# Kernel tuning notes

Hardware: AMD Instinct MI355X
Metric: run time of the kernel (lower is better)

## Reference

```python
import jax, jax.numpy as jnp
import numpy as np
from jax import lax

N_RAYS, N_STEPS, G = 4096, 160, 160
COLOR_DIM, WIDTH = 3, 128
POS_PE, VIEW_PE = 5, 4
XYZ_MIN, XYZ_MAX = -1.0, 1.0
NEAR = 0.05
STEPSIZE = 0.5
VOXEL_SIZE = (XYZ_MAX - XYZ_MIN) / G
DIST = STEPSIZE * VOXEL_SIZE
S_VAL = 80.0
FASTCOLOR_THRES = 1e-7
MASK_THRES = 1e-3
ALPHA_INIT = 1e-4
ACT_SHIFT = float(np.log(1.0 / (1.0 - ALPHA_INIT) - 1.0))
SMOOTH_K, SMOOTH_SIGMA = 5, 1.0
POSFREQ = jnp.asarray([2.0 ** i for i in range(POS_PE)], jnp.float32)
VIEWFREQ = jnp.asarray([2.0 ** i for i in range(VIEW_PE)], jnp.float32)


def _gauss_kernel():
    ax = np.arange(SMOOTH_K) - SMOOTH_K // 2
    g = np.exp(-(ax ** 2) / (2.0 * SMOOTH_SIGMA ** 2))
    k = g[:, None, None] * g[None, :, None] * g[None, None, :]
    return jnp.asarray(k / k.sum(), np.float32)[None, None]


def _trilerp(grid, pts):
    # grid [C,Gx,Gx,Gx]; pts [...,3] in world coords -> [..., C] (align_corners trilinear)
    Gx = grid.shape[-1]
    u = (pts - XYZ_MIN) / (XYZ_MAX - XYZ_MIN) * (Gx - 1)
    u = jnp.clip(u, 0.0, Gx - 1.0)
    i0 = jnp.clip(jnp.floor(u).astype(jnp.int32), 0, Gx - 2)
    f = u - i0.astype(u.dtype)
    x0, y0, z0 = i0[..., 0], i0[..., 1], i0[..., 2]
    fx, fy, fz = f[..., 0], f[..., 1], f[..., 2]
    def g8(ix, iy, iz):
        return grid[:, ix, iy, iz]  # [C, ...]
    out = (g8(x0, y0, z0) * (1 - fx) * (1 - fy) * (1 - fz)
         + g8(x0, y0, z0 + 1) * (1 - fx) * (1 - fy) * fz
         + g8(x0, y0 + 1, z0) * (1 - fx) * fy * (1 - fz)
         + g8(x0, y0 + 1, z0 + 1) * (1 - fx) * fy * fz
         + g8(x0 + 1, y0, z0) * fx * (1 - fy) * (1 - fz)
         + g8(x0 + 1, y0, z0 + 1) * fx * (1 - fy) * fz
         + g8(x0 + 1, y0 + 1, z0) * fx * fy * (1 - fz)
         + g8(x0 + 1, y0 + 1, z0 + 1) * fx * fy * fz)
    return jnp.moveaxis(out, 0, -1)


def _alphas2weights(alpha):
    # per-ray (segmented) exclusive cumprod of transmittance; alpha [N,S]
    T = jnp.cumprod(1.0 - alpha, axis=1)
    T_excl = jnp.concatenate([jnp.ones_like(T[:, :1]), T[:, :-1]], axis=1)
    return alpha * T_excl, T[:, -1]


def _mlp(x, w0, b0, w1, b1, w2, b2):
    h = jax.nn.relu(x @ w0 + b0)
    h = jax.nn.relu(h @ w1 + b1)
    return h @ w2 + b2


def _forward(rays_o, rays_d, viewdirs, sdf_grid, mask_density,
             off_color_grid, emo_color_grid,
             off_w0, off_b0, off_w1, off_b1, off_w2, off_b2,
             emo_w0, emo_b0, emo_w1, emo_b1, emo_w2, emo_b2, em_modes):
    N = rays_o.shape[0]
    t = NEAR + DIST * jnp.arange(N_STEPS, dtype=jnp.float32)
    ray_pts = rays_o[:, None, :] + rays_d[:, None, :] * t[None, :, None]  # [N,S,3]

    # MaskCache: threshold alpha from coarse density grid (boolean keep mask)
    dens = _trilerp(mask_density, ray_pts)[..., 0]
    mask_alpha = 1.0 - jnp.exp(-jax.nn.softplus(dens + ACT_SHIFT) * DIST)
    keep0 = mask_alpha >= MASK_THRES  # [N,S]

    # Gaussian-smoothed SDF grid + central-difference gradient grid
    sdf_s = lax.conv_general_dilated(sdf_grid, _gauss_kernel(), (1, 1, 1), 'SAME',
                                     dimension_numbers=('NCDHW', 'OIDHW', 'NCDHW'))[0]  # [1,G,G,G]
    s = sdf_s[0]
    grad_grid = jnp.zeros((3, G, G, G), sdf_grid.dtype)
    grad_grid = grad_grid.at[0, 1:-1].set((s[2:] - s[:-2]) / (2 * VOXEL_SIZE))
    grad_grid = grad_grid.at[1, :, 1:-1].set((s[:, 2:] - s[:, :-2]) / (2 * VOXEL_SIZE))
    grad_grid = grad_grid.at[2, :, :, 1:-1].set((s[:, :, 2:] - s[:, :, :-2]) / (2 * VOXEL_SIZE))

    sdf = _trilerp(sdf_s, ray_pts)[..., 0]   # [N,S]
    gradient = _trilerp(grad_grid, ray_pts)  # [N,S,3]

    # NeuS alpha from sdf (scatter, grad variant, cos_anneal = 1)
    true_cos = jnp.einsum('nd,nsd->ns', viewdirs, gradient)
    iter_cos = -jax.nn.relu(-true_cos)
    prev_cdf = jax.nn.sigmoid((sdf - iter_cos * DIST * 0.5) * S_VAL)
    next_cdf = jax.nn.sigmoid((sdf + iter_cos * DIST * 0.5) * S_VAL)
    alpha = jnp.clip((prev_cdf - next_cdf + 1e-5) / (prev_cdf + 1e-5), 0.0, 1.0)
    alpha = jnp.where(keep0, alpha, 0.0)  # masked points contribute nothing

    weights, _ = _alphas2weights(alpha)
    keep1 = weights > FASTCOLOR_THRES
    alpha = jnp.where(keep1, alpha, 0.0)
    weights, alphainv_last = _alphas2weights(alpha)

    # features: pos PE, view PE (per-ray, gathered by ray_id == broadcast), normal
    rays_xyz = (ray_pts - XYZ_MIN) / (XYZ_MAX - XYZ_MIN)  # [N,S,3]
    xyz_emb = (rays_xyz[..., None] * POSFREQ).reshape(N, N_STEPS, -1)
    v_emb = (viewdirs[..., None] * VIEWFREQ).reshape(N, -1)
    v_full = jnp.concatenate([v_emb, jnp.sin(v_emb), jnp.cos(v_emb)], -1)
    v_full = jnp.broadcast_to(v_full[:, None, :], (N, N_STEPS, v_full.shape[-1]))
    normal = gradient / (jnp.linalg.norm(gradient, axis=-1, keepdims=True) + 1e-5)
    rgb_feat = jnp.concatenate([rays_xyz, jnp.sin(xyz_emb), jnp.cos(xyz_emb), v_full, normal], -1)

    off_in = jnp.concatenate([_trilerp(off_color_grid, ray_pts), rgb_feat], -1)
    emo_in = jnp.concatenate([_trilerp(emo_color_grid, ray_pts), rgb_feat], -1)
    off_rgb = jax.nn.sigmoid(_mlp(off_in, off_w0, off_b0, off_w1, off_b1, off_w2, off_b2))
    emo_rgb = jax.nn.sigmoid(_mlp(emo_in, emo_w0, emo_b0, emo_w1, emo_b1, emo_w2, emo_b2))
    on_mask = (em_modes == 1)[:, None, None]  # em_modes[ray_id] == 1
    rgb = jnp.where(on_mask, emo_rgb, 0.0) + off_rgb

    w_ = weights[..., None]
    rgb_marched = jnp.sum(w_ * rgb, axis=1)  # segment_coo(sum over ray_id)
    cum_weights = jnp.sum(w_, axis=1)        # [N,1]
    return rgb_marched, alphainv_last, 1.0 - cum_weights


def setup_inputs() -> dict:
    key = jax.random.key(0)
    ks = jax.random.split(key, 12)
    rays_o = jax.random.uniform(ks[0], (N_RAYS, 3), jnp.float32, -0.3, 0.3)
    rd = jax.random.normal(ks[1], (N_RAYS, 3), jnp.float32)
    rays_d = rd / jnp.linalg.norm(rd, axis=-1, keepdims=True)
    viewdirs = rays_d
    em_modes = jax.random.randint(ks[2], (N_RAYS,), 0, 2)
    lin = np.linspace(-1.0, 1.0, G, dtype=np.float32)
    x, y, z = np.meshgrid(lin, lin, lin, indexing='ij')
    sdf_grid = jnp.asarray(np.sqrt(x ** 2 + y ** 2 + z ** 2) - 1.0)[None, None]  # sphere-SDF init
    mask_density = jax.random.normal(ks[3], (1, 80, 80, 80), jnp.float32) * 2.0 + 12.0
    off_color_grid = jax.random.normal(ks[4], (COLOR_DIM, G, G, G), jnp.float32) * 0.1
    emo_color_grid = jax.random.normal(ks[5], (COLOR_DIM, G, G, G), jnp.float32) * 0.1
    DIM0 = 3 + 3 * POS_PE * 2 + 3 * VIEW_PE * 3 + COLOR_DIM + 3  # = 75
    def lw(k, i, o):
        return jax.random.normal(k, (i, o), jnp.float32) * (1.0 / np.sqrt(i))
    return dict(rays_o=rays_o, rays_d=rays_d, viewdirs=viewdirs, em_modes=em_modes,
                sdf_grid=sdf_grid, mask_density=mask_density,
                off_color_grid=off_color_grid, emo_color_grid=emo_color_grid,
                off_w0=lw(ks[6], DIM0, WIDTH), off_b0=jnp.zeros((WIDTH,), jnp.float32),
                off_w1=lw(ks[7], WIDTH, WIDTH), off_b1=jnp.zeros((WIDTH,), jnp.float32),
                off_w2=lw(ks[8], WIDTH, 3), off_b2=jnp.zeros((3,), jnp.float32),
                emo_w0=lw(ks[9], DIM0, WIDTH), emo_b0=jnp.zeros((WIDTH,), jnp.float32),
                emo_w1=lw(ks[10], WIDTH, WIDTH), emo_b1=jnp.zeros((WIDTH,), jnp.float32),
                emo_w2=lw(ks[11], WIDTH, 3), emo_b2=jnp.zeros((3,), jnp.float32))


def reference(rays_o, rays_d, viewdirs, em_modes, sdf_grid, mask_density,
              off_color_grid, emo_color_grid,
              off_w0, off_b0, off_w1, off_b1, off_w2, off_b2,
              emo_w0, emo_b0, emo_w1, emo_b1, emo_w2, emo_b2):
    return _forward(rays_o, rays_d, viewdirs, sdf_grid, mask_density,
                    off_color_grid, emo_color_grid,
                    off_w0, off_b0, off_w1, off_b1, off_w2, off_b2,
                    emo_w0, emo_b0, emo_w1, emo_b1, emo_w2, emo_b2, em_modes)
```

## Files before the change

### kernel.cpp

```cpp
#include <hip/hip_runtime.h>

#define NRAYS 4096
#define NSTEPS 160
#define NSAMP (NRAYS*NSTEPS)
#define GG 160
#define GG2 (GG*GG)
#define GG3 (GG*GG2)
#define GM 80
#define GM2 (GM*GM)

#define NEARV 0.05f
#define DISTV 0.00625f
#define SVAL 80.0f
#define ACT_SHIFT_C (-9.2102403669758813f)
#define INV2H 40.0f
#define MASK_THRES_C 1e-3f
#define FAST_THRES_C 1e-7f

#define KW0 0.05448868454964295f
#define KW1 0.24420134200323332f
#define KW2 0.40261994689424750f

__device__ __forceinline__ float sigmf(float x){ return 1.0f/(1.0f+__expf(-x)); }
__device__ __forceinline__ float softplusf_(float x){ return (x>20.0f)? x : log1pf(__expf(x)); }

__device__ __forceinline__ void tricoord(float p, int Gx, int& i0, float& fr){
  float u = (p + 1.0f)*0.5f*(float)(Gx-1);
  u = fminf(fmaxf(u, 0.0f), (float)(Gx-1));
  int i = (int)floorf(u);
  i = min(max(i,0), Gx-2);
  i0 = i; fr = u - (float)i;
}

__global__ __launch_bounds__(256) void ksmooth_yz(const float* __restrict__ in, float* __restrict__ out,
                                                  float* __restrict__ outbuf, int* __restrict__ cnt){
  __shared__ float S[36][37];
  __shared__ float Tz[36][33];
  const int bx = blockIdx.x;
  const int t = threadIdx.x;
  if (bx == 0){
    for (int i = t; i < NRAYS*3; i += 256) outbuf[i] = 0.0f;
    if (t < 2) cnt[t] = 0;
  }
  const int x  = bx / 25;
  const int tile = bx % 25;
  const int Y0 = (tile/5)*32, Z0 = (tile%5)*32;
  const float kw[5] = {KW0,KW1,KW2,KW1,KW0};
  for (int i = t; i < 36*36; i += 256){
    int r = i/36, c = i - (i/36)*36;
    int y = Y0 + r - 2, z = Z0 + c - 2;
    float v = 0.0f;
    if (y>=0 && y<GG && z>=0 && z<GG) v = in[(x*GG+y)*GG+z];
    S[r][c] = v;
  }
  __syncthreads();
  for (int i = t; i < 36*32; i += 256){
    int r = i >> 5, c = i & 31;
    float acc = 0.f;
    #pragma unroll
    for (int d=0; d<5; d++) acc += kw[d]*S[r][c+d];
    Tz[r][c] = acc;
  }
  __syncthreads();
  for (int i = t; i < 32*32; i += 256){
    int yy = i >> 5, c = i & 31;
    float acc = 0.f;
    #pragma unroll
    for (int d=0; d<5; d++) acc += kw[d]*Tz[yy+d][c];
    out[(x*GG + Y0+yy)*GG + Z0 + c] = acc;
  }
}

__global__ __launch_bounds__(64) void kmarch(
  const float* __restrict__ ro, const float* __restrict__ rd,
  const float* __restrict__ vd, const int* __restrict__ em,
  const float* __restrict__ maskg, const float* __restrict__ Y,
  int* __restrict__ slist, float* __restrict__ sw, float* __restrict__ sgrad,
  int* __restrict__ cnt, float* __restrict__ out)
{
  int n = blockIdx.x*64 + threadIdx.x;
  if (n >= NRAYS) return;
  const float ox=ro[n*3+0], oy=ro[n*3+1], oz=ro[n*3+2];
  const float dx=rd[n*3+0], dy=rd[n*3+1], dz=rd[n*3+2];
  const float vx=vd[n*3+0], vy=vd[n*3+1], vz=vd[n*3+2];
  const int emn = em[n];
  const float kwc[5] = {KW0,KW1,KW2,KW1,KW0};
  float T1=1.0f, T2=1.0f, cum=0.0f;
  for (int s=0; s<NSTEPS; s++){
    float tt = NEARV + DISTV*(float)s;
    float px = ox + dx*tt, py = oy + dy*tt, pz = oz + dz*tt;

    int mx,my,mz; float mfx,mfy,mfz;
    tricoord(px, GM, mx, mfx); tricoord(py, GM, my, mfy); tricoord(pz, GM, mz, mfz);
    int mid = (mx*GM + my)*GM + mz;
    float d000=maskg[mid],        d001=maskg[mid+1];
    float d010=maskg[mid+GM],     d011=maskg[mid+GM+1];
    float d100=maskg[mid+GM2],    d101=maskg[mid+GM2+1];
    float d110=maskg[mid+GM2+GM], d111=maskg[mid+GM2+GM+1];
    float m00 = d000 + (d001-d000)*mfz;
    float m01 = d010 + (d011-d010)*mfz;
    float m10 = d100 + (d101-d100)*mfz;
    float m11 = d110 + (d111-d110)*mfz;
    float m0 = m00 + (m01-m00)*mfy;
    float m1 = m10 + (m11-m10)*mfy;
    float dens = m0 + (m1-m0)*mfx;
    float malpha = 1.0f - __expf(-softplusf_(dens + ACT_SHIFT_C)*DISTV);

    int ix,iy,iz; float fx,fy,fz;
    tricoord(px, GG, ix, fx); tricoord(py, GG, iy, fy); tricoord(pz, GG, iz, fz);

    float R[2][2][8];
    #pragma unroll
    for (int jb=0;jb<2;jb++)
      #pragma unroll
      for (int jc=0;jc<2;jc++)
        #pragma unroll
        for (int j=0;j<8;j++){
          int a = ix-3+j;
          R[jb][jc][j] = (a>=0 && a<GG) ? Y[(a*GG + iy+jb)*GG + iz+jc] : 0.0f;
        }
    const bool hasym = (iy>=1), hasyp = (iy<=GG-3);
    const bool haszm = (iz>=1), haszp = (iz<=GG-3);
    float Eym[2][6], Eyp[2][6], Ezm[2][6], Ezp[2][6];
    #pragma unroll
    for (int jc=0;jc<2;jc++)
      #pragma unroll
      for (int j=0;j<6;j++){
        int a = ix-2+j;
        bool ax = (a>=0 && a<GG);
        Eym[jc][j] = (hasym && ax) ? Y[(a*GG + iy-1)*GG + iz+jc] : 0.0f;
        Eyp[jc][j] = (hasyp && ax) ? Y[(a*GG + iy+2)*GG + iz+jc] : 0.0f;
      }
    #pragma unroll
    for (int jb=0;jb<2;jb++)
      #pragma unroll
      for (int j=0;j<6;j++){
        int a = ix-2+j;
        bool ax = (a>=0 && a<GG);
        Ezm[jb][j] = (haszm && ax) ? Y[(a*GG + iy+jb)*GG + iz-1] : 0.0f;
        Ezp[jb][j] = (haszp && ax) ? Y[(a*GG + iy+jb)*GG + iz+2] : 0.0f;
      }

    float sdf=0.0f, gx=0.0f, gy=0.0f, gz=0.0f;
    #pragma unroll
    for (int ja=0;ja<2;ja++){
      #pragma unroll
      for (int jb=0;jb<2;jb++){
        #pragma unroll
        for (int jc=0;jc<2;jc++){
          float w = (ja?fx:1.0f-fx)*(jb?fy:1.0f-fy)*(jc?fz:1.0f-fz);
          const float* r = R[jb][jc];
          float s0=0.0f;
          #pragma unroll
          for (int t2=0;t2<5;t2++) s0 += kwc[t2]*r[ja+1+t2];
          sdf += w*s0;
          int a = ix+ja, b = iy+jb, c = iz+jc;
          if (a>=1 && a<=GG-2){
            float sp=0.0f, sm=0.0f;
            #pragma unroll
            for (int t2=0;t2<5;t2++){ sp += kwc[t2]*r[ja+2+t2]; sm += kwc[t2]*r[ja+t2]; }
            gx += w*INV2H*(sp-sm);
          }
          if (b>=1 && b<=GG-2){
            float acc=0.0f;
            if (jb==0){
              const float* up = R[1][jc];
              const float* dn = Eym[jc];
              #pragma unroll
              for (int t2=0;t2<5;t2++) acc += kwc[t2]*(up[ja+1+t2] - dn[ja+t2]);
            } else {
              const float* up = Eyp[jc];
              const float* dn = R[0][jc];
              #pragma unroll
              for (int t2=0;t2<5;t2++) acc += kwc[t2]*(up[ja+t2] - dn[ja+1+t2]);
            }
            gy += w*INV2H*acc;
          }
          if (c>=1 && c<=GG-2){
            float acc=0.0f;
            if (jc==0){
              const float* up = R[jb][1];
              const float* dn = Ezm[jb];
              #pragma unroll
              for (int t2=0;t2<5;t2++) acc += kwc[t2]*(up[ja+1+t2] - dn[ja+t2]);
            } else {
              const float* up = Ezp[jb];
              const float* dn = R[jb][0];
              #pragma unroll
              for (int t2=0;t2<5;t2++) acc += kwc[t2]*(up[ja+t2] - dn[ja+1+t2]);
            }
            gz += w*INV2H*acc;
          }
        }
      }
    }

    float tc = vx*gx + vy*gy + vz*gz;
    float icos = fminf(tc, 0.0f);
    float e = icos*DISTV*0.5f;
    float prev = sigmf((sdf - e)*SVAL);
    float nxt  = sigmf((sdf + e)*SVAL);
    float alpha = (prev - nxt + 1e-5f)/(prev + 1e-5f);
    alpha = fminf(fmaxf(alpha, 0.0f), 1.0f);
    if (!(malpha >= MASK_THRES_C)) alpha = 0.0f;

    float w1 = alpha*T1; T1 *= (1.0f - alpha);
    float a2 = (w1 > FAST_THRES_C) ? alpha : 0.0f;
    float wv = a2*T2;   T2 *= (1.0f - a2);
    cum += wv;
    if (wv > 0.0f){
      int pos;
      if (emn == 1){ int p = atomicAdd(&cnt[1], 1); pos = NSAMP - 1 - p; }
      else         { pos = atomicAdd(&cnt[0], 1); }
      slist[pos] = n*NSTEPS + s;
      sw[pos] = wv;
      sgrad[pos*3+0]=gx; sgrad[pos*3+1]=gy; sgrad[pos*3+2]=gz;
    }
    if (T1 <= FAST_THRES_C) break;
  }
  out[NRAYS*3 + n] = T2;
  out[NRAYS*4 + n] = 1.0f - cum;
}

#define DO4(ACC, XV) \
  ACC.x += XV.x*w0.x; ACC.y += XV.x*w0.y; ACC.z += XV.x*w0.z; ACC.w += XV.x*w0.w; \
  ACC.x += XV.y*w1.x; ACC.y += XV.y*w1.y; ACC.z += XV.y*w1.z; ACC.w += XV.y*w1.w; \
  ACC.x += XV.z*w2.x; ACC.y += XV.z*w2.y; ACC.z += XV.z*w2.z; ACC.w += XV.z*w2.w; \
  ACC.x += XV.w*w3.x; ACC.y += XV.w*w3.y; ACC.z += XV.w*w3.z; ACC.w += XV.w*w3.w;

__global__ __launch_bounds__(256, 1) void kmlp8(
  const float* __restrict__ ro, const float* __restrict__ rd,
  const float* __restrict__ vd,
  const float* __restrict__ offc, const float* __restrict__ emoc,
  const int* __restrict__ slist, const float* __restrict__ sw,
  const float* __restrict__ sgrad, const int* __restrict__ cnt,
  const float* __restrict__ W0o, const float* __restrict__ b0o,
  const float* __restrict__ W1o, const float* __restrict__ b1o,
  const float* __restrict__ W2o, const float* __restrict__ b2o,
  const float* __restrict__ W0e, const float* __restrict__ b0e,
  const float* __restrict__ W1e, const float* __restrict__ b1e,
  const float* __restrict__ W2e, const float* __restrict__ b2e,
  float* __restrict__ out)
{
  __shared__ float X [4][8][80];
  __shared__ float HA[4][8][128];
  __shared__ float HB[4][8][128];
  __shared__ float SW_[4][8];
  __shared__ int   SS_[4][8];

  const int t = threadIdx.x;
  const int wid = t >> 6;
  const int lt  = t & 63;
  const int c0 = cnt[0], c1 = cnt[1];
  const int seg1 = NSAMP - c1;
  const int totOff = c0 + c1;
  const int nOff = (totOff + 7) >> 3;
  const int nEmo = (c1 + 7) >> 3;
  const int nTask = nOff + nEmo;

  for (int task = blockIdx.x*4 + wid; task < nTask; task += gridDim.x*4) {
    const int head = (task >= nOff) ? 1 : 0;
    const int total = head ? c1 : totOff;
    const int base = (head ? (task - nOff) : task) * 8;

    const float* W0 = head ? W0e : W0o;  const float* b0 = head ? b0e : b0o;
    const float* W1 = head ? W1e : W1o;  const float* b1 = head ? b1e : b1o;
    const float* W2 = head ? W2e : W2o;  const float* b2 = head ? b2e : b2o;
    const float* cg = head ? emoc : offc;
    const float4* W04 = (const float4*)W0;
    const float4* W14 = (const float4*)W1;

    {
      const int s = lt >> 3;
      const int r = lt & 7;
      int v = base + s;
      bool vld = (v < total);
      int vc = vld ? v : (total > 0 ? total - 1 : 0);
      int gi = head ? (seg1 + vc) : ((vc < c0) ? vc : seg1 + (vc - c0));
      const int samp = slist[gi];
      if (r == 0){
        SS_[wid][s] = samp;
        SW_[wid][s] = vld ? sw[gi] : 0.0f;
      }
      const int n = samp / NSTEPS;
      const int step = samp - n*NSTEPS;
      const float tt = NEARV + DISTV*(float)step;
      const float px = ro[n*3+0] + rd[n*3+0]*tt;
      const float py = ro[n*3+1] + rd[n*3+1]*tt;
      const float pz = ro[n*3+2] + rd[n*3+2]*tt;
      float* Xs = X[wid][s];
      if (r < 3) {
        int ix,iy,iz; float fx,fy,fz;
        tricoord(px, GG, ix, fx); tricoord(py, GG, iy, fy); tricoord(pz, GG, iz, fz);
        const float* g = cg + (size_t)r * GG3;
        const int id = (ix*GG + iy)*GG + iz;
        float v000=g[id],        v001=g[id+1];
        float v010=g[id+GG],     v011=g[id+GG+1];
        float v100=g[id+GG2],    v101=g[id+GG2+1];
        float v110=g[id+GG2+GG], v111=g[id+GG2+GG+1];
        float c00 = v000 + (v001-v000)*fz;
        float c01 = v010 + (v011-v010)*fz;
        float c10 = v100 + (v101-v100)*fz;
        float c11 = v110 + (v111-v110)*fz;
        float cl0 = c00 + (c01-c00)*fy;
        float cl1 = c10 + (c11-c10)*fy;
        Xs[r] = cl0 + (cl1-cl0)*fx;
      } else if (r == 3) {
        Xs[3] = (px+1.0f)*0.5f;
        Xs[4] = (py+1.0f)*0.5f;
        Xs[5] = (pz+1.0f)*0.5f;
        float gx = sgrad[gi*3+0], gy = sgrad[gi*3+1], gz = sgrad[gi*3+2];
        float inv = 1.0f/(sqrtf(gx*gx+gy*gy+gz*gz)+1e-5f);
        Xs[72] = gx*inv; Xs[73] = gy*inv; Xs[74] = gz*inv;
        Xs[75] = 0.0f; Xs[76] = 0.0f; Xs[77] = 0.0f; Xs[78] = 0.0f; Xs[79] = 0.0f;
      } else if (r < 7) {
        const int a = r - 4;
        const float coord = (a==0)?px:((a==1)?py:pz);
        const float rxyz = (coord+1.0f)*0.5f;
        float fr = 1.0f;
        #pragma unroll
        for (int q = 0; q < 5; q++) {
          float e = rxyz*fr; fr *= 2.0f;
          Xs[6  + a*5 + q] = __sinf(e);
          Xs[21 + a*5 + q] = __cosf(e);
        }
      } else {
        #pragma unroll
        for (int a = 0; a < 3; a++){
          const float vv = vd[n*3+a];
          float fr = 1.0f;
          #pragma unroll
          for (int q = 0; q < 4; q++) {
            float e = vv*fr; fr *= 2.0f;
            Xs[36 + a*4 + q] = e;
            Xs[48 + a*4 + q] = __sinf(e);
            Xs[60 + a*4 + q] = __cosf(e);
          }
        }
      }
    }

    const int sme = lt >> 5;
    const int l32 = lt & 31;
    const int sb = sme*4;

    {
      const float4 bb = ((const float4*)b0)[l32];
      float4 a0 = bb, a1 = bb, a2 = bb, a3 = bb;
      const float* X0 = X[wid][sb+0];
      const float* X1 = X[wid][sb+1];
      const float* X2 = X[wid][sb+2];
      const float* X3 = X[wid][sb+3];
      #pragma unroll 2
      for (int k4 = 0; k4 < 72; k4 += 4){
        float4 w0 = W04[(k4+0)*32 + l32];
        float4 w1 = W04[(k4+1)*32 + l32];
        float4 w2 = W04[(k4+2)*32 + l32];
        float4 w3 = W04[(k4+3)*32 + l32];
        float4 x0 = *(const float4*)&X0[k4];
        float4 x1 = *(const float4*)&X1[k4];
        float4 x2 = *(const float4*)&X2[k4];
        float4 x3 = *(const float4*)&X3[k4];
        DO4(a0, x0); DO4(a1, x1); DO4(a2, x2); DO4(a3, x3);
      }
      #pragma unroll
      for (int k = 72; k < 75; k++){
        float4 w = W04[k*32 + l32];
        float x0 = X0[k], x1 = X1[k], x2 = X2[k], x3 = X3[k];
        a0.x+=x0*w.x; a0.y+=x0*w.y; a0.z+=x0*w.z; a0.w+=x0*w.w;
        a1.x+=x1*w.x; a1.y+=x1*w.y; a1.z+=x1*w.z; a1.w+=x1*w.w;
        a2.x+=x2*w.x; a2.y+=x2*w.y; a2.z+=x2*w.z; a2.w+=x2*w.w;
        a3.x+=x3*w.x; a3.y+=x3*w.y; a3.z+=x3*w.z; a3.w+=x3*w.w;
      }
      a0.x=fmaxf(a0.x,0.f); a0.y=fmaxf(a0.y,0.f); a0.z=fmaxf(a0.z,0.f); a0.w=fmaxf(a0.w,0.f);
      a1.x=fmaxf(a1.x,0.f); a1.y=fmaxf(a1.y,0.f); a1.z=fmaxf(a1.z,0.f); a1.w=fmaxf(a1.w,0.f);
      a2.x=fmaxf(a2.x,0.f); a2.y=fmaxf(a2.y,0.f); a2.z=fmaxf(a2.z,0.f); a2.w=fmaxf(a2.w,0.f);
      a3.x=fmaxf(a3.x,0.f); a3.y=fmaxf(a3.y,0.f); a3.z=fmaxf(a3.z,0.f); a3.w=fmaxf(a3.w,0.f);
      *(float4*)&HA[wid][sb+0][l32*4] = a0;
      *(float4*)&HA[wid][sb+1][l32*4] = a1;
      *(float4*)&HA[wid][sb+2][l32*4] = a2;
      *(float4*)&HA[wid][sb+3][l32*4] = a3;
    }

    {
      const float4 bb = ((const float4*)b1)[l32];
      float4 a0 = bb, a1 = bb, a2 = bb, a3 = bb;
      const float* H0 = HA[wid][sb+0];
      const float* H1 = HA[wid][sb+1];
      const float* H2p = HA[wid][sb+2];
      const float* H3 = HA[wid][sb+3];
      #pragma unroll 2
      for (int k4 = 0; k4 < 128; k4 += 4){
        float4 w0 = W14[(k4+0)*32 + l32];
        float4 w1 = W14[(k4+1)*32 + l32];
        float4 w2 = W14[(k4+2)*32 + l32];
        float4 w3 = W14[(k4+3)*32 + l32];
        float4 x0 = *(const float4*)&H0[k4];
        float4 x1 = *(const float4*)&H1[k4];
        float4 x2 = *(const float4*)&H2p[k4];
        float4 x3 = *(const float4*)&H3[k4];
        DO4(a0, x0); DO4(a1, x1); DO4(a2, x2); DO4(a3, x3);
      }
      a0.x=fmaxf(a0.x,0.f); a0.y=fmaxf(a0.y,0.f); a0.z=fmaxf(a0.z,0.f); a0.w=fmaxf(a0.w,0.f);
      a1.x=fmaxf(a1.x,0.f); a1.y=fmaxf(a1.y,0.f); a1.z=fmaxf(a1.z,0.f); a1.w=fmaxf(a1.w,0.f);
      a2.x=fmaxf(a2.x,0.f); a2.y=fmaxf(a2.y,0.f); a2.z=fmaxf(a2.z,0.f); a2.w=fmaxf(a2.w,0.f);
      a3.x=fmaxf(a3.x,0.f); a3.y=fmaxf(a3.y,0.f); a3.z=fmaxf(a3.z,0.f); a3.w=fmaxf(a3.w,0.f);
      *(float4*)&HB[wid][sb+0][l32*4] = a0;
      *(float4*)&HB[wid][sb+1][l32*4] = a1;
      *(float4*)&HB[wid][sb+2][l32*4] = a2;
      *(float4*)&HB[wid][sb+3][l32*4] = a3;
    }

    {
      float W2r[4][3];
      #pragma unroll
      for (int q = 0; q < 4; q++){
        W2r[q][0] = W2[(l32*4+q)*3+0];
        W2r[q][1] = W2[(l32*4+q)*3+1];
        W2r[q][2] = W2[(l32*4+q)*3+2];
      }
      #pragma unroll
      for (int m = 0; m < 4; m++){
        const int s = sb + m;
        float4 h = *(const float4*)&HB[wid][s][l32*4];
        float c0v = h.x*W2r[0][0] + h.y*W2r[1][0] + h.z*W2r[2][0] + h.w*W2r[3][0];
        float c1v = h.x*W2r[0][1] + h.y*W2r[1][1] + h.z*W2r[2][1] + h.w*W2r[3][1];
        float c2v = h.x*W2r[0][2] + h.y*W2r[1][2] + h.z*W2r[2][2] + h.w*W2r[3][2];
        #pragma unroll
        for (int d=16; d>=1; d>>=1){
          c0v += __shfl_down(c0v, d, 32);
          c1v += __shfl_down(c1v, d, 32);
          c2v += __shfl_down(c2v, d, 32);
        }
        if (l32 == 0){
          float w = SW_[wid][s];
          if (w > 0.0f){
            int n2 = SS_[wid][s] / NSTEPS;
            atomicAdd(&out[n2*3+0], w * sigmf(c0v + b2[0]));
            atomicAdd(&out[n2*3+1], w * sigmf(c1v + b2[1]));
            atomicAdd(&out[n2*3+2], w * sigmf(c2v + b2[2]));
          }
        }
      }
    }
  }
}

extern "C" void kernel_launch(void* const* d_in, const int* in_sizes, int n_in,
                              void* d_out, int out_size, void* d_ws, size_t ws_size,
                              hipStream_t stream) {
  const float* ro    = (const float*)d_in[0];
  const float* rd    = (const float*)d_in[1];
  const float* vd    = (const float*)d_in[2];
  const int*   em    = (const int*)d_in[3];
  const float* sdfg  = (const float*)d_in[4];
  const float* maskg = (const float*)d_in[5];
  const float* offc  = (const float*)d_in[6];
  const float* emoc  = (const float*)d_in[7];
  const float* W0o = (const float*)d_in[8];
  const float* b0o = (const float*)d_in[9];
  const float* W1o = (const float*)d_in[10];
  const float* b1o = (const float*)d_in[11];
  const float* W2o = (const float*)d_in[12];
  const float* b2o = (const float*)d_in[13];
  const float* W0e = (const float*)d_in[14];
  const float* b0e = (const float*)d_in[15];
  const float* W1e = (const float*)d_in[16];
  const float* b1e = (const float*)d_in[17];
  const float* W2e = (const float*)d_in[18];
  const float* b2e = (const float*)d_in[19];

  float* out = (float*)d_out;
  float* ws  = (float*)d_ws;
  float* Yb    = ws;
  float* swb   = ws + GG3;
  float* sgradb= swb + NSAMP;
  int*   slist = (int*)(sgradb + 3*(size_t)NSAMP);
  int*   cnt   = slist + NSAMP;

  ksmooth_yz<<<GG*25, 256, 0, stream>>>(sdfg, Yb, out, cnt);

  kmarch<<<NRAYS/64, 64, 0, stream>>>(ro, rd, vd, em, maskg, Yb,
                                      slist, swb, sgradb, cnt, out);

  kmlp8<<<256, 256, 0, stream>>>(ro, rd, vd, offc, emoc,
                                 slist, swb, sgradb, cnt,
                                 W0o,b0o,W1o,b1o,W2o,b2o,
                                 W0e,b0e,W1e,b1e,W2e,b2e, out);
}
```

Baseline: 54.32 us.

## March each ray with a full wavefront, distributing stencil loads across lanes

The ray-march kernel now assigns one 64-lane wavefront per ray instead of one thread per ray. Each lane fetches one of the ~88 smoothed-SDF stencil values or one of the 8 mask-grid corners and computes a partial weighted contribution. Five butterfly shuffle reductions then combine the sdf, gradient and density terms. This exposes far more parallelism: 4096 rays previously gave only 64 blocks of 64 threads. The cost is serial per-step shuffle reductions and 64x redundant scalar transmittance logic per ray.

Result: slower. 87.74 us (+61.5%).

```diff
diff --git a/kernel.cpp b/kernel.cpp
--- a/kernel.cpp
+++ b/kernel.cpp
@@ -23,6 +23,12 @@
 
 __device__ __forceinline__ float sigmf(float x){ return 1.0f/(1.0f+__expf(-x)); }
 __device__ __forceinline__ float softplusf_(float x){ return (x>20.0f)? x : log1pf(__expf(x)); }
+
+__device__ __forceinline__ float kwf(int i){
+  float r = 0.0f;
+  r = (i==0)?KW0:r; r=(i==1)?KW1:r; r=(i==2)?KW2:r; r=(i==3)?KW1:r; r=(i==4)?KW0:r;
+  return r;
+}
 
 __device__ __forceinline__ void tricoord(float p, int Gx, int& i0, float& fr){
   float u = (p + 1.0f)*0.5f*(float)(Gx-1);
@@ -71,155 +77,137 @@
   }
 }
 
-__global__ __launch_bounds__(64) void kmarch(
+__global__ __launch_bounds__(256) void kmarch_wave(
   const float* __restrict__ ro, const float* __restrict__ rd,
   const float* __restrict__ vd, const int* __restrict__ em,
   const float* __restrict__ maskg, const float* __restrict__ Y,
   int* __restrict__ slist, float* __restrict__ sw, float* __restrict__ sgrad,
   int* __restrict__ cnt, float* __restrict__ out)
 {
-  int n = blockIdx.x*64 + threadIdx.x;
+  const int t = threadIdx.x;
+  const int l = t & 63;
+  const int n = blockIdx.x*4 + (t>>6);
   if (n >= NRAYS) return;
+
   const float ox=ro[n*3+0], oy=ro[n*3+1], oz=ro[n*3+2];
   const float dx=rd[n*3+0], dy=rd[n*3+1], dz=rd[n*3+2];
   const float vx=vd[n*3+0], vy=vd[n*3+1], vz=vd[n*3+2];
   const int emn = em[n];
-  const float kwc[5] = {KW0,KW1,KW2,KW1,KW0};
+
+  const bool isR = (l < 32);
+  const bool isE = (l >= 32 && l < 56);
+  const bool isM = (l >= 56);
+  const int r_jb = (l>>4)&1, r_jc = (l>>3)&1, r_u = l&7;
+  const int e1 = l-32, e_wh = e1/12, e_r = e1%12, e_jc = e_r/6, e_u = e_r%6;
+  const int mb = l-56, m_ca=(mb>>2)&1, m_cb=(mb>>1)&1, m_cc=mb&1;
+  const bool isZ = (l < 24);
+  const int z_wh = l/12, z_r = l%12, z_jb = z_r/6, z_u = z_r%6;
+
+  const float kA = kwf(r_u-1), kB = kwf(r_u-2), kC = kwf(r_u), kD = kwf(r_u-3);
+  const float dG1 = kB - kC, dG2 = kD - kA;
+  const float kE = kwf(e_u), kF = kwf(e_u-1);
+  const float kZ1 = kwf(z_u), kZ2 = kwf(z_u-1);
+
   float T1=1.0f, T2=1.0f, cum=0.0f;
   for (int s=0; s<NSTEPS; s++){
-    float tt = NEARV + DISTV*(float)s;
-    float px = ox + dx*tt, py = oy + dy*tt, pz = oz + dz*tt;
+    const float tt = NEARV + DISTV*(float)s;
+    const float px = ox + dx*tt, py = oy + dy*tt, pz = oz + dz*tt;
 
     int mx,my,mz; float mfx,mfy,mfz;
     tricoord(px, GM, mx, mfx); tricoord(py, GM, my, mfy); tricoord(pz, GM, mz, mfz);
-    int mid = (mx*GM + my)*GM + mz;
-    float d000=maskg[mid],        d001=maskg[mid+1];
-    float d010=maskg[mid+GM],     d011=maskg[mid+GM+1];
-    float d100=maskg[mid+GM2],    d101=maskg[mid+GM2+1];
-    float d110=maskg[mid+GM2+GM], d111=maskg[mid+GM2+GM+1];
-    float m00 = d000 + (d001-d000)*mfz;
-    float m01 = d010 + (d011-d010)*mfz;
-    float m10 = d100 + (d101-d100)*mfz;
-    float m11 = d110 + (d111-d110)*mfz;
-    float m0 = m00 + (m01-m00)*mfy;
-    float m1 = m10 + (m11-m10)*mfy;
-    float dens = m0 + (m1-m0)*mfx;
-    float malpha = 1.0f - __expf(-softplusf_(dens + ACT_SHIFT_C)*DISTV);
-
     int ix,iy,iz; float fx,fy,fz;
     tricoord(px, GG, ix, fx); tricoord(py, GG, iy, fy); tricoord(pz, GG, iz, fz);
 
-    float R[2][2][8];
+    const float ax0 = (ix>=1)?1.f:0.f, ax1 = (ix<=GG-3)?1.f:0.f;
+    const float by0f = (iy>=1)?1.f:0.f, by1f = (iy<=GG-3)?1.f:0.f;
+    const float bz0f = (iz>=1)?1.f:0.f, bz1f = (iz<=GG-3)?1.f:0.f;
+    const float wx0=1.f-fx, wx1=fx, wy0=1.f-fy, wy1=fy, wz0=1.f-fz, wz1=fz;
+
+    float V1 = 0.0f, V2 = 0.0f;
+    if (isR){
+      int a = ix-3+r_u;
+      if (a>=0 && a<GG) V1 = Y[(a*GG + iy+r_jb)*GG + iz+r_jc];
+    } else if (isE){
+      int a = ix-2+e_u;
+      int b = e_wh ? (iy+2) : (iy-1);
+      bool ok = (a>=0 && a<GG) && (e_wh ? (iy<=GG-3) : (iy>=1));
+      if (ok) V1 = Y[(a*GG + b)*GG + iz+e_jc];
+    } else {
+      V1 = maskg[((mx+m_ca)*GM + my+m_cb)*GM + mz+m_cc];
+    }
+    if (isZ){
+      int a = ix-2+z_u;
+      int c = z_wh ? (iz+2) : (iz-1);
+      bool ok = (a>=0 && a<GG) && (z_wh ? (iz<=GG-3) : (iz>=1));
+      if (ok) V2 = Y[(a*GG + iy+z_jb)*GG + c];
+    }
+
+    float p_sdf=0.f, p_gx=0.f, p_gy=0.f, p_gz=0.f, p_den=0.f;
+    if (isR){
+      const float wyv = r_jb ? wy1 : wy0;
+      const float wzv = r_jc ? wz1 : wz0;
+      const float cxs = wx0*kA + wx1*kB;
+      const float cgx = wx0*ax0*dG1 + wx1*ax1*dG2;
+      const float base = wzv*cxs*INV2H*V1;
+      p_sdf = wyv*wzv*cxs*V1;
+      p_gx  = wyv*wzv*cgx*V1*INV2H;
+      p_gy  = base * (r_jb ? (wy0*by0f) : -(wy1*by1f));
+      p_gz  = wyv*cxs*INV2H*V1 * (r_jc ? (wz0*bz0f) : -(wz1*bz1f));
+    } else if (isE){
+      const float wzv = e_jc ? wz1 : wz0;
+      const float cxe = wx0*kE + wx1*kF;
+      const float gyw = e_wh ? (wy1*by1f) : -(wy0*by0f);
+      p_gy = wzv*cxe*INV2H*gyw*V1;
+    } else {
+      const float wmx = m_ca? mfx : 1.f-mfx;
+      const float wmy = m_cb? mfy : 1.f-mfy;
+      const float wmz = m_cc? mfz : 1.f-mfz;
+      p_den = wmx*wmy*wmz*V1;
+    }
+    if (isZ){
+      const float wyv = z_jb ? wy1 : wy0;
+      const float cxe2 = wx0*kZ1 + wx1*kZ2;
+      const float gzw = z_wh ? (wz1*bz1f) : -(wz0*bz0f);
+      p_gz += wyv*cxe2*INV2H*gzw*V2;
+    }
+
     #pragma unroll
-    for (int jb=0;jb<2;jb++)
-      #pragma unroll
-      for (int jc=0;jc<2;jc++)
-        #pragma unroll
-        for (int j=0;j<8;j++){
-          int a = ix-3+j;
-          R[jb][jc][j] = (a>=0 && a<GG) ? Y[(a*GG + iy+jb)*GG + iz+jc] : 0.0f;
-        }
-    const bool hasym = (iy>=1), hasyp = (iy<=GG-3);
-    const bool haszm = (iz>=1), haszp = (iz<=GG-3);
-    float Eym[2][6], Eyp[2][6], Ezm[2][6], Ezp[2][6];
-    #pragma unroll
-    for (int jc=0;jc<2;jc++)
-      #pragma unroll
-      for (int j=0;j<6;j++){
-        int a = ix-2+j;
-        bool ax = (a>=0 && a<GG);
-        Eym[jc][j] = (hasym && ax) ? Y[(a*GG + iy-1)*GG + iz+jc] : 0.0f;
-        Eyp[jc][j] = (hasyp && ax) ? Y[(a*GG + iy+2)*GG + iz+jc] : 0.0f;
-      }
-    #pragma unroll
-    for (int jb=0;jb<2;jb++)
-      #pragma unroll
-      for (int j=0;j<6;j++){
-        int a = ix-2+j;
-        bool ax = (a>=0 && a<GG);
-        Ezm[jb][j] = (haszm && ax) ? Y[(a*GG + iy+jb)*GG + iz-1] : 0.0f;
-        Ezp[jb][j] = (haszp && ax) ? Y[(a*GG + iy+jb)*GG + iz+2] : 0.0f;
-      }
-
-    float sdf=0.0f, gx=0.0f, gy=0.0f, gz=0.0f;
-    #pragma unroll
-    for (int ja=0;ja<2;ja++){
-      #pragma unroll
-      for (int jb=0;jb<2;jb++){
-        #pragma unroll
-        for (int jc=0;jc<2;jc++){
-          float w = (ja?fx:1.0f-fx)*(jb?fy:1.0f-fy)*(jc?fz:1.0f-fz);
-          const float* r = R[jb][jc];
-          float s0=0.0f;
-          #pragma unroll
-          for (int t2=0;t2<5;t2++) s0 += kwc[t2]*r[ja+1+t2];
-          sdf += w*s0;
-          int a = ix+ja, b = iy+jb, c = iz+jc;
-          if (a>=1 && a<=GG-2){
-            float sp=0.0f, sm=0.0f;
-            #pragma unroll
-            for (int t2=0;t2<5;t2++){ sp += kwc[t2]*r[ja+2+t2]; sm += kwc[t2]*r[ja+t2]; }
-            gx += w*INV2H*(sp-sm);
-          }
-          if (b>=1 && b<=GG-2){
-            float acc=0.0f;
-            if (jb==0){
-              const float* up = R[1][jc];
-              const float* dn = Eym[jc];
-              #pragma unroll
-              for (int t2=0;t2<5;t2++) acc += kwc[t2]*(up[ja+1+t2] - dn[ja+t2]);
-            } else {
-              const float* up = Eyp[jc];
-              const float* dn = R[0][jc];
-              #pragma unroll
-              for (int t2=0;t2<5;t2++) acc += kwc[t2]*(up[ja+t2] - dn[ja+1+t2]);
-            }
-            gy += w*INV2H*acc;
-          }
-          if (c>=1 && c<=GG-2){
-            float acc=0.0f;
-            if (jc==0){
-              const float* up = R[jb][1];
-              const float* dn = Ezm[jb];
-              #pragma unroll
-              for (int t2=0;t2<5;t2++) acc += kwc[t2]*(up[ja+1+t2] - dn[ja+t2]);
-            } else {
-              const float* up = Ezp[jb];
-              const float* dn = R[jb][0];
-              #pragma unroll
-              for (int t2=0;t2<5;t2++) acc += kwc[t2]*(up[ja+t2] - dn[ja+1+t2]);
-            }
-            gz += w*INV2H*acc;
-          }
-        }
-      }
-    }
-
-    float tc = vx*gx + vy*gy + vz*gz;
-    float icos = fminf(tc, 0.0f);
-    float e = icos*DISTV*0.5f;
-    float prev = sigmf((sdf - e)*SVAL);
-    float nxt  = sigmf((sdf + e)*SVAL);
+    for (int d=1; d<64; d<<=1){
+      p_sdf += __shfl_xor(p_sdf, d, 64);
+      p_gx  += __shfl_xor(p_gx , d, 64);
+      p_gy  += __shfl_xor(p_gy , d, 64);
+      p_gz  += __shfl_xor(p_gz , d, 64);
+      p_den += __shfl_xor(p_den, d, 64);
+    }
+
+    const float malpha = 1.0f - __expf(-softplusf_(p_den + ACT_SHIFT_C)*DISTV);
+    const float tc = vx*p_gx + vy*p_gy + vz*p_gz;
+    const float icos = fminf(tc, 0.0f);
+    const float e = icos*DISTV*0.5f;
+    const float prev = sigmf((p_sdf - e)*SVAL);
+    const float nxt  = sigmf((p_sdf + e)*SVAL);
     float alpha = (prev - nxt + 1e-5f)/(prev + 1e-5f);
     alpha = fminf(fmaxf(alpha, 0.0f), 1.0f);
     if (!(malpha >= MASK_THRES_C)) alpha = 0.0f;
 
-    float w1 = alpha*T1; T1 *= (1.0f - alpha);
-    float a2 = (w1 > FAST_THRES_C) ? alpha : 0.0f;
-    float wv = a2*T2;   T2 *= (1.0f - a2);
+    const float w1 = alpha*T1; T1 *= (1.0f - alpha);
+    const float a2 = (w1 > FAST_THRES_C) ? alpha : 0.0f;
+    const float wv = a2*T2;   T2 *= (1.0f - a2);
     cum += wv;
-    if (wv > 0.0f){
+    if (wv > 0.0f && l == 0){
       int pos;
       if (emn == 1){ int p = atomicAdd(&cnt[1], 1); pos = NSAMP - 1 - p; }
       else         { pos = atomicAdd(&cnt[0], 1); }
       slist[pos] = n*NSTEPS + s;
       sw[pos] = wv;
-      sgrad[pos*3+0]=gx; sgrad[pos*3+1]=gy; sgrad[pos*3+2]=gz;
+      sgrad[pos*3+0]=p_gx; sgrad[pos*3+1]=p_gy; sgrad[pos*3+2]=p_gz;
     }
     if (T1 <= FAST_THRES_C) break;
   }
-  out[NRAYS*3 + n] = T2;
-  out[NRAYS*4 + n] = 1.0f - cum;
+  if (l == 0){
+    out[NRAYS*3 + n] = T2;
+    out[NRAYS*4 + n] = 1.0f - cum;
+  }
 }
 
 #define DO4(ACC, XV) \
@@ -480,8 +468,8 @@
 
   ksmooth_yz<<<GG*25, 256, 0, stream>>>(sdfg, Yb, out, cnt);
 
-  kmarch<<<NRAYS/64, 64, 0, stream>>>(ro, rd, vd, em, maskg, Yb,
-                                      slist, swb, sgradb, cnt, out);
+  kmarch_wave<<<NRAYS/4, 256, 0, stream>>>(ro, rd, vd, em, maskg, Yb,
+                                           slist, swb, sgradb, cnt, out);
 
   kmlp8<<<256, 256, 0, stream>>>(ro, rd, vd, offc, emoc,
                                  slist, swb, sgradb, cnt,
```
